# Optimization experiments

Measured on AMD Instinct MI355X. Metric: run time of the kernel, lower is better.

## Reference

```python
import jax, jax.numpy as jnp
import numpy as np

HID = 256
NP_ = 100
KS = 3
EPS = 1e-5


def setup_inputs() -> dict:
    key = jax.random.key(0)
    k1, k2, k3, k4 = jax.random.split(key, 4)
    B = 1024
    f = jax.random.normal(k1, (B, NP_, HID), dtype=jnp.float32)
    k = jax.random.normal(k2, (B, NP_, HID), dtype=jnp.float32)
    W_lin = jax.random.normal(k3, (HID, NP_ * KS), dtype=jnp.float32) / np.sqrt(HID)
    b_lin = jax.random.normal(k4, (NP_ * KS,), dtype=jnp.float32) * 0.01
    gamma = jnp.ones((HID,), dtype=jnp.float32)
    beta = jnp.zeros((HID,), dtype=jnp.float32)
    return {"f": f, "k": k, "W_lin": W_lin, "b_lin": b_lin, "gamma": gamma, "beta": beta}


def reference(f, k, W_lin, b_lin, gamma, beta):
    B, P, L = k.shape  # [B, 100, 256]
    # dynamic conv weights: [B, out=100, in=100, T=3]
    w = (jnp.einsum('bph,ho->bpo', f, W_lin) + b_lin).reshape(B, P, P, KS)
    # 'same' padding for kernel 3 -> pad 1 each side along L
    kp = jnp.pad(k, ((0, 0), (0, 0), (1, 1)))
    # shifted views: [B, in, L, T] (cross-correlation, as torch conv1d)
    ks = jnp.stack([kp[:, :, t:t + L] for t in range(KS)], axis=-1)
    out = jnp.einsum('boct,bclt->bol', w, ks)  # [B, 100, 256]
    # LayerNorm over last dim
    mu = jnp.mean(out, axis=-1, keepdims=True)
    var = jnp.mean((out - mu) ** 2, axis=-1, keepdims=True)
    return (out - mu) / jnp.sqrt(var + EPS) * gamma + beta
```

## Files before the change

### kernel.cpp

```cpp
#include <hip/hip_runtime.h>
#include <hip/hip_bf16.h>

#define HID   256
#define NP    100
#define KSZ   3
#define NPKS  (NP*KSZ)
#define K2PAD 384
#define N1T   24
#define PC    104
#define KTROWS 258
#define KT_ELEMS (KTROWS*PC + 80)
#define WS_PITCH 40
#define WS_ELEMS (112*WS_PITCH)

using bf16x8 = __attribute__((ext_vector_type(8))) short;
using f32x4  = __attribute__((ext_vector_type(4))) float;

__device__ __forceinline__ short f2bf(float x) {
    __hip_bfloat16 h = __float2bfloat16(x);
    return __builtin_bit_cast(short, h);
}

__global__ void dyconv_prep(const float* __restrict__ W_lin,
                            const float* __restrict__ b_lin,
                            short* __restrict__ W2f,
                            float* __restrict__ b2f) {
    int gid = blockIdx.x * blockDim.x + threadIdx.x;
    int lane = gid & 63;
    int ent  = gid >> 6;
    int kt = ent / N1T;
    int nt = ent % N1T;
    int n  = nt*16 + (lane & 15);
    int t  = n >> 7;
    int c  = n & 127;
    int k0 = kt*32 + ((lane >> 4) << 3);
    short vals[8];
#pragma unroll
    for (int j = 0; j < 8; ++j) {
        float v = (c < NP) ? W_lin[(k0 + j) * NPKS + c*KSZ + t] : 0.0f;
        vals[j] = f2bf(v);
    }
    *reinterpret_cast<bf16x8*>(&W2f[(size_t)gid * 8]) =
        *reinterpret_cast<bf16x8*>(vals);
    if (gid < K2PAD) {
        int tt = gid >> 7, cc = gid & 127;
        b2f[gid] = (cc < NP) ? b_lin[cc*KSZ + tt] : 0.0f;
    }
}

__global__ __launch_bounds__(256, 2)
void dyconv_gemm1(const float* __restrict__ f, const short* __restrict__ W2f,
                  const float* __restrict__ b2f, short* __restrict__ w2, int Mrows) {
    const int tid = threadIdx.x, wave = tid>>6, lane = tid&63, lg = lane>>4, li = lane&15;
    const int r0 = blockIdx.x * 128;

    bf16x8 a1[2][8];
#pragma unroll
    for (int mi = 0; mi < 2; ++mi) {
        int myr = r0 + (wave*2 + mi)*16 + li; if (myr > Mrows-1) myr = Mrows-1;
        const float* frow = f + (size_t)myr * HID + lg*8;
#pragma unroll
        for (int kt = 0; kt < 8; ++kt) {
            float4 u = *reinterpret_cast<const float4*>(frow + kt*32);
            float4 v = *reinterpret_cast<const float4*>(frow + kt*32 + 4);
            short tmp[8] = {f2bf(u.x),f2bf(u.y),f2bf(u.z),f2bf(u.w),
                            f2bf(v.x),f2bf(v.y),f2bf(v.z),f2bf(v.w)};
            a1[mi][kt] = *reinterpret_cast<bf16x8*>(tmp);
        }
    }

    const short* Wl = W2f + (size_t)lane * 8;
    const int prow0 = lg*4;

#pragma unroll 1
    for (int q = 0; q < 4; ++q) {
        const int nb = q*6;
        f32x4 acc[2][6];
#pragma unroll
        for (int mi = 0; mi < 2; ++mi)
#pragma unroll
            for (int i = 0; i < 6; ++i) acc[mi][i] = (f32x4){0.f,0.f,0.f,0.f};

        bf16x8 F0[8], F1[8];
#define LDW(FB, NTL) { _Pragma("unroll") for (int kt = 0; kt < 8; ++kt) \
    FB[kt] = *reinterpret_cast<const bf16x8*>(Wl + ((size_t)(kt*N1T + nb + (NTL)) << 9)); }
#define MM2(FB, NTL) { _Pragma("unroll") for (int kt = 0; kt < 8; ++kt) { \
    acc[0][NTL] = __builtin_amdgcn_mfma_f32_16x16x32_bf16(a1[0][kt], FB[kt], acc[0][NTL], 0,0,0); \
    acc[1][NTL] = __builtin_amdgcn_mfma_f32_16x16x32_bf16(a1[1][kt], FB[kt], acc[1][NTL], 0,0,0); } }
        LDW(F0,0)  LDW(F1,1)
        MM2(F0,0)  LDW(F0,2)
        MM2(F1,1)  LDW(F1,3)
        MM2(F0,2)  LDW(F0,4)
        MM2(F1,3)  LDW(F1,5)
        MM2(F0,4)
        MM2(F1,5)
#undef LDW
#undef MM2

#pragma unroll
        for (int mi = 0; mi < 2; ++mi) {
#pragma unroll
            for (int r = 0; r < 4; ++r) {
                int gr = r0 + (wave*2 + mi)*16 + prow0 + r;
                if (gr < Mrows) {
                    int bb = gr / NP, p = gr % NP;
                    short* wrow = w2 + ((size_t)bb*12*NP + p)*32;
#pragma unroll
                    for (int ntl = 0; ntl < 6; ++ntl) {
                        int nt = nb + ntl;
                        float bias = b2f[nt*16 + li];
                        wrow[(size_t)(nt>>1)*NP*32 + (nt&1)*16 + li] =
                            f2bf(acc[mi][ntl][r] + bias);
                    }
                }
            }
        }
    }
}

__global__ __launch_bounds__(256, 2)
void dyconv_conv(const float* __restrict__ k, const short* __restrict__ w2,
                 const float* __restrict__ gamma, const float* __restrict__ beta,
                 float* __restrict__ out) {
    __shared__ short kT[KT_ELEMS];
    float* lnbuf = reinterpret_cast<float*>(kT);

    const int b = blockIdx.x, tid = threadIdx.x;
    const int wave = tid>>6, lane = tid&63, lg = lane>>4, li = lane&15;

    if (tid < 52) {
        *reinterpret_cast<unsigned int*>(&kT[tid*2]) = 0u;
        *reinterpret_cast<unsigned int*>(&kT[257*PC + tid*2]) = 0u;
    }
    *reinterpret_cast<unsigned long long*>(&kT[(tid+1)*PC + 100]) = 0ull;
    if (tid < 20)
        *reinterpret_cast<unsigned long long*>(&kT[KTROWS*PC + tid*4]) = 0ull;

    const float* kb = k + (size_t)b * (NP*HID);
    for (int u = tid; u < (NP/2)*HID; u += 256) {
        int c2 = u >> 8;
        int l  = u & 255;
        int c  = c2*2;
        float v0 = kb[(size_t)c*HID + l];
        float v1 = kb[(size_t)(c+1)*HID + l];
        unsigned int pk = (unsigned int)(unsigned short)f2bf(v0)
                        | ((unsigned int)(unsigned short)f2bf(v1) << 16);
        *reinterpret_cast<unsigned int*>(&kT[(l+1)*PC + c]) = pk;
    }

    f32x4 acc2[7][4];
#pragma unroll
    for (int mt = 0; mt < 7; ++mt)
#pragma unroll
        for (int j = 0; j < 4; ++j) acc2[mt][j] = (f32x4){0.f,0.f,0.f,0.f};

    const short* wb = w2 + (size_t)b * 12 * NP * 32;
    const short* wp[7];
#pragma unroll
    for (int mt = 0; mt < 7; ++mt) {
        int p = mt*16 + li; if (p > NP-1) p = NP-1;
        wp[mt] = wb + (size_t)p*32 + lg*8;
    }

    __syncthreads();

    bf16x8 a2[7], a2n[7];
#pragma unroll
    for (int mt = 0; mt < 7; ++mt)
        a2[mt] = *reinterpret_cast<const bf16x8*>(wp[mt]);

#pragma unroll
    for (int kc = 0; kc < 12; ++kc) {
        if (kc < 11) {
#pragma unroll
            for (int mt = 0; mt < 7; ++mt)
                a2n[mt] = *reinterpret_cast<const bf16x8*>(wp[mt] + (size_t)(kc+1)*NP*32);
        }
        int k2 = kc*32 + lg*8;
        int t  = k2 >> 7, c = k2 & 127;
#pragma unroll
        for (int j = 0; j < 4; ++j) {
            int l = (wave*4 + j)*16 + li;
            bf16x8 b2v = *reinterpret_cast<const bf16x8*>(&kT[(l + t)*PC + c]);
#pragma unroll
            for (int mt = 0; mt < 7; ++mt)
                acc2[mt][j] = __builtin_amdgcn_mfma_f32_16x16x32_bf16(
                    a2[mt], b2v, acc2[mt][j], 0,0,0);
        }
#pragma unroll
        for (int mt = 0; mt < 7; ++mt) a2[mt] = a2n[mt];
    }

    __syncthreads();

    float* psum  = lnbuf;
    float* mrstd = lnbuf + 4*112*2;
#pragma unroll
    for (int mt = 0; mt < 7; ++mt) {
#pragma unroll
        for (int r = 0; r < 4; ++r) {
            float s1 = 0.f, s2 = 0.f;
#pragma unroll
            for (int j = 0; j < 4; ++j) {
                float v = acc2[mt][j][r];
                s1 += v; s2 += v*v;
            }
#pragma unroll
            for (int m = 1; m < 16; m <<= 1) {
                s1 += __shfl_xor(s1, m, 64);
                s2 += __shfl_xor(s2, m, 64);
            }
            if (li == 0) {
                int p = mt*16 + lg*4 + r;
                psum[(wave*112 + p)*2 + 0] = s1;
                psum[(wave*112 + p)*2 + 1] = s2;
            }
        }
    }
    __syncthreads();
    if (tid < 112) {
        float S1 = 0.f, S2 = 0.f;
#pragma unroll
        for (int w2i = 0; w2i < 4; ++w2i) {
            S1 += psum[(w2i*112 + tid)*2 + 0];
            S2 += psum[(w2i*112 + tid)*2 + 1];
        }
        float mean = S1 * (1.0f/HID);
        float var  = S2 * (1.0f/HID) - mean*mean;
        mrstd[tid*2 + 0] = mean;
        mrstd[tid*2 + 1] = rsqrtf(var + 1e-5f);
    }
    __syncthreads();

    float* ob = out + (size_t)b * (NP*HID);
#pragma unroll
    for (int j = 0; j < 4; ++j) {
        int l = (wave*4 + j)*16 + li;
        float g  = gamma[l];
        float be = beta[l];
#pragma unroll
        for (int mt = 0; mt < 7; ++mt) {
#pragma unroll
            for (int r = 0; r < 4; ++r) {
                int p = mt*16 + lg*4 + r;
                if (p < NP) {
                    float mean = mrstd[p*2], rstd = mrstd[p*2 + 1];
                    ob[p*HID + l] = (acc2[mt][j][r] - mean)*rstd*g + be;
                }
            }
        }
    }
}

__global__ __launch_bounds__(256)
void dyconv_main(const float* __restrict__ f, const float* __restrict__ k,
                 const short* __restrict__ W2f, const float* __restrict__ b2f,
                 const float* __restrict__ gamma, const float* __restrict__ beta,
                 float* __restrict__ out) {
    __shared__ short kT[KT_ELEMS];
    __shared__ short wS[WS_ELEMS];
    float* lnbuf = reinterpret_cast<float*>(wS);
    const int b = blockIdx.x, tid = threadIdx.x;
    const int wave = tid>>6, lane = tid&63, lg = lane>>4, li = lane&15;
    for (int i = tid; i < KT_ELEMS/8; i += 256)
        reinterpret_cast<int4*>(kT)[i] = make_int4(0,0,0,0);
    __syncthreads();
    const float* kb = k + (size_t)b * (NP*HID);
    for (int idx = tid; idx < NP*HID; idx += 256) {
        int c = idx >> 8, l = idx & 255;
        kT[(l+1)*PC + c] = f2bf(kb[idx]);
    }
    const float* fb = f + (size_t)b * (NP*HID);
    const int nmy = (wave < 3) ? 2 : 1;
    bf16x8 a1[2][8];
#pragma unroll
    for (int mi = 0; mi < 2; ++mi) {
        if (mi < nmy) {
            int mt = wave + 4*mi;
            int p  = mt*16 + li; if (p > NP-1) p = NP-1;
            const float* rowp = fb + (size_t)p * HID + lg*8;
#pragma unroll
            for (int kt = 0; kt < 8; ++kt) {
                float4 u = *reinterpret_cast<const float4*>(rowp + kt*32);
                float4 v = *reinterpret_cast<const float4*>(rowp + kt*32 + 4);
                short tmp[8] = {f2bf(u.x),f2bf(u.y),f2bf(u.z),f2bf(u.w),
                                f2bf(v.x),f2bf(v.y),f2bf(v.z),f2bf(v.w)};
                a1[mi][kt] = *reinterpret_cast<bf16x8*>(tmp);
            }
        }
    }
    f32x4 acc2[7][4];
#pragma unroll
    for (int mt = 0; mt < 7; ++mt)
#pragma unroll
        for (int j = 0; j < 4; ++j) acc2[mt][j] = (f32x4){0.f,0.f,0.f,0.f};
    __syncthreads();
    for (int kc = 0; kc < 12; ++kc) {
        f32x4 acc1[2][2];
#pragma unroll
        for (int mi = 0; mi < 2; ++mi)
#pragma unroll
            for (int n = 0; n < 2; ++n) acc1[mi][n] = (f32x4){0.f,0.f,0.f,0.f};
#pragma unroll
        for (int kt = 0; kt < 8; ++kt) {
            bf16x8 b1[2];
#pragma unroll
            for (int ntl = 0; ntl < 2; ++ntl) {
                int NT = kc*2 + ntl;
                b1[ntl] = *reinterpret_cast<const bf16x8*>(
                    &W2f[(((size_t)kt*N1T + NT)*64 + lane)*8]);
            }
#pragma unroll
            for (int mi = 0; mi < 2; ++mi) {
                if (mi < nmy) {
                    acc1[mi][0] = __builtin_amdgcn_mfma_f32_16x16x32_bf16(
                        a1[mi][kt], b1[0], acc1[mi][0], 0,0,0);
                    acc1[mi][1] = __builtin_amdgcn_mfma_f32_16x16x32_bf16(
                        a1[mi][kt], b1[1], acc1[mi][1], 0,0,0);
                }
            }
        }
#pragma unroll
        for (int mi = 0; mi < 2; ++mi) {
            if (mi < nmy) {
                int mt = wave + 4*mi;
#pragma unroll
                for (int ntl = 0; ntl < 2; ++ntl) {
                    int col  = ntl*16 + li;
                    float bias = b2f[kc*32 + col];
#pragma unroll
                    for (int r = 0; r < 4; ++r) {
                        int row = mt*16 + lg*4 + r;
                        wS[row*WS_PITCH + col] = f2bf(acc1[mi][ntl][r] + bias);
                    }
                }
            }
        }
        __syncthreads();
        bf16x8 a2[7];
#pragma unroll
        for (int mt = 0; mt < 7; ++mt)
            a2[mt] = *reinterpret_cast<const bf16x8*>(&wS[(mt*16 + li)*WS_PITCH + lg*8]);
        int k2 = kc*32 + lg*8;
        int t  = k2 >> 7, c = k2 & 127;
#pragma unroll
        for (int j = 0; j < 4; ++j) {
            int l = (wave*4 + j)*16 + li;
            bf16x8 b2v = *reinterpret_cast<const bf16x8*>(&kT[(l + t)*PC + c]);
#pragma unroll
            for (int mt = 0; mt < 7; ++mt)
                acc2[mt][j] = __builtin_amdgcn_mfma_f32_16x16x32_bf16(
                    a2[mt], b2v, acc2[mt][j], 0,0,0);
        }
        __syncthreads();
    }
    float* psum  = lnbuf;
    float* mrstd = lnbuf + 4*112*2;
#pragma unroll
    for (int mt = 0; mt < 7; ++mt) {
#pragma unroll
        for (int r = 0; r < 4; ++r) {
            float s1 = 0.f, s2 = 0.f;
#pragma unroll
            for (int j = 0; j < 4; ++j) {
                float v = acc2[mt][j][r];
                s1 += v; s2 += v*v;
            }
#pragma unroll
            for (int m = 1; m < 16; m <<= 1) {
                s1 += __shfl_xor(s1, m, 64);
                s2 += __shfl_xor(s2, m, 64);
            }
            if (li == 0) {
                int p = mt*16 + lg*4 + r;
                psum[(wave*112 + p)*2 + 0] = s1;
                psum[(wave*112 + p)*2 + 1] = s2;
            }
        }
    }
    __syncthreads();
    if (tid < 112) {
        float S1 = 0.f, S2 = 0.f;
#pragma unroll
        for (int w2i = 0; w2i < 4; ++w2i) {
            S1 += psum[(w2i*112 + tid)*2 + 0];
            S2 += psum[(w2i*112 + tid)*2 + 1];
        }
        float mean = S1 * (1.0f/HID);
        float var  = S2 * (1.0f/HID) - mean*mean;
        mrstd[tid*2 + 0] = mean;
        mrstd[tid*2 + 1] = rsqrtf(var + 1e-5f);
    }
    __syncthreads();
    float* ob = out + (size_t)b * (NP*HID);
#pragma unroll
    for (int j = 0; j < 4; ++j) {
        int l = (wave*4 + j)*16 + li;
        float g  = gamma[l];
        float be = beta[l];
#pragma unroll
        for (int mt = 0; mt < 7; ++mt) {
#pragma unroll
            for (int r = 0; r < 4; ++r) {
                int p = mt*16 + lg*4 + r;
                if (p < NP) {
                    float mean = mrstd[p*2], rstd = mrstd[p*2 + 1];
                    ob[p*HID + l] = (acc2[mt][j][r] - mean)*rstd*g + be;
                }
            }
        }
    }
}

extern "C" void kernel_launch(void* const* d_in, const int* in_sizes, int n_in,
                              void* d_out, int out_size, void* d_ws, size_t ws_size,
                              hipStream_t stream) {
    const float* f     = (const float*)d_in[0];
    const float* k     = (const float*)d_in[1];
    const float* W_lin = (const float*)d_in[2];
    const float* b_lin = (const float*)d_in[3];
    const float* gamma = (const float*)d_in[4];
    const float* beta  = (const float*)d_in[5];
    float* out = (float*)d_out;

    short* W2f = (short*)d_ws;
    float* b2f = (float*)((char*)d_ws + 196608);
    const size_t off_w2 = 198144;
    const int B = in_sizes[0] / (NP*HID);
    const int Mrows = B * NP;
    const size_t need = off_w2 + (size_t)B * 12 * NP * 32 * 2;

    dyconv_prep<<<48, 256, 0, stream>>>(W_lin, b_lin, W2f, b2f);

    if (ws_size >= need) {
        short* w2 = (short*)((char*)d_ws + off_w2);
        dyconv_gemm1<<<(Mrows + 127)/128, 256, 0, stream>>>(f, W2f, b2f, w2, Mrows);
        dyconv_conv<<<B, 256, 0, stream>>>(k, w2, gamma, beta, out);
    } else {
        dyconv_main<<<B, 256, 0, stream>>>(f, k, W2f, b2f, gamma, beta, out);
    }
}
```

Baseline: 175.2 us.

## Stage GEMM1 weight tiles in LDS via double-buffered global_load_lds

```diff
diff --git a/kernel.cpp b/kernel.cpp
--- a/kernel.cpp
+++ b/kernel.cpp
@@ -48,9 +48,10 @@
     }
 }
 
-__global__ __launch_bounds__(256, 2)
+__global__ __launch_bounds__(256, 3)
 void dyconv_gemm1(const float* __restrict__ f, const short* __restrict__ W2f,
                   const float* __restrict__ b2f, short* __restrict__ w2, int Mrows) {
+    __shared__ short wlds[2][24*512];
     const int tid = threadIdx.x, wave = tid>>6, lane = tid&63, lg = lane>>4, li = lane&15;
     const int r0 = blockIdx.x * 128;
 
@@ -69,33 +70,48 @@
         }
     }
 
-    const short* Wl = W2f + (size_t)lane * 8;
+#define STAGE(BUF, C) { _Pragma("unroll") for (int i = 0; i < 6; ++i) { \
+        int fi = wave*6 + i; \
+        int ntl = fi >> 3, kt = fi & 7; \
+        int nt = (C)*3 + ntl; \
+        const short* gsrc = &W2f[(((size_t)(kt*N1T + nt))*64 + lane)*8]; \
+        __builtin_amdgcn_global_load_lds( \
+            (const __attribute__((address_space(1))) unsigned int*)gsrc, \
+            (__attribute__((address_space(3))) unsigned int*)&wlds[BUF][fi*512], \
+            16, 0, 0); } }
+
     const int prow0 = lg*4;
 
+    STAGE(0, 0)
+    __syncthreads();
+
 #pragma unroll 1
-    for (int q = 0; q < 4; ++q) {
-        const int nb = q*6;
-        f32x4 acc[2][6];
+    for (int c = 0; c < 8; ++c) {
+        if (c < 7) STAGE((c+1)&1, c+1)
+
+        const short* lbase = wlds[c&1];
+        f32x4 acc[2][3];
 #pragma unroll
         for (int mi = 0; mi < 2; ++mi)
 #pragma unroll
-            for (int i = 0; i < 6; ++i) acc[mi][i] = (f32x4){0.f,0.f,0.f,0.f};
-
-        bf16x8 F0[8], F1[8];
-#define LDW(FB, NTL) { _Pragma("unroll") for (int kt = 0; kt < 8; ++kt) \
-    FB[kt] = *reinterpret_cast<const bf16x8*>(Wl + ((size_t)(kt*N1T + nb + (NTL)) << 9)); }
-#define MM2(FB, NTL) { _Pragma("unroll") for (int kt = 0; kt < 8; ++kt) { \
-    acc[0][NTL] = __builtin_amdgcn_mfma_f32_16x16x32_bf16(a1[0][kt], FB[kt], acc[0][NTL], 0,0,0); \
-    acc[1][NTL] = __builtin_amdgcn_mfma_f32_16x16x32_bf16(a1[1][kt], FB[kt], acc[1][NTL], 0,0,0); } }
-        LDW(F0,0)  LDW(F1,1)
-        MM2(F0,0)  LDW(F0,2)
-        MM2(F1,1)  LDW(F1,3)
-        MM2(F0,2)  LDW(F0,4)
-        MM2(F1,3)  LDW(F1,5)
-        MM2(F0,4)
-        MM2(F1,5)
-#undef LDW
-#undef MM2
+            for (int i = 0; i < 3; ++i) acc[mi][i] = (f32x4){0.f,0.f,0.f,0.f};
+
+#pragma unroll
+        for (int ntl = 0; ntl < 3; ++ntl) {
+#pragma unroll
+            for (int kt = 0; kt < 8; ++kt) {
+                bf16x8 bfr = *reinterpret_cast<const bf16x8*>(
+                    lbase + (ntl*8 + kt)*512 + lane*8);
+                acc[0][ntl] = __builtin_amdgcn_mfma_f32_16x16x32_bf16(
+                    a1[0][kt], bfr, acc[0][ntl], 0,0,0);
+                acc[1][ntl] = __builtin_amdgcn_mfma_f32_16x16x32_bf16(
+                    a1[1][kt], bfr, acc[1][ntl], 0,0,0);
+            }
+        }
+
+        float bias[3];
+#pragma unroll
+        for (int ntl = 0; ntl < 3; ++ntl) bias[ntl] = b2f[(c*3 + ntl)*16 + li];
 
 #pragma unroll
         for (int mi = 0; mi < 2; ++mi) {
@@ -106,16 +122,17 @@
                     int bb = gr / NP, p = gr % NP;
                     short* wrow = w2 + ((size_t)bb*12*NP + p)*32;
 #pragma unroll
-                    for (int ntl = 0; ntl < 6; ++ntl) {
-                        int nt = nb + ntl;
-                        float bias = b2f[nt*16 + li];
+                    for (int ntl = 0; ntl < 3; ++ntl) {
+                        int nt = c*3 + ntl;
                         wrow[(size_t)(nt>>1)*NP*32 + (nt&1)*16 + li] =
-                            f2bf(acc[mi][ntl][r] + bias);
+                            f2bf(acc[mi][ntl][r] + bias[ntl]);
                     }
                 }
             }
         }
-    }
+        __syncthreads();
+    }
+#undef STAGE
 }
 
 __global__ __launch_bounds__(256, 2)
```

Measured after the change: 156.9 us. -10.5%, faster.
